# Kernel optimization log

Hardware: AMD Instinct MI355X
Metric: run time of the kernel (lower is better)

Reference implementation:

```python
import jax, jax.numpy as jnp
import numpy as np


def setup_inputs() -> dict:
    key = jax.random.key(0)
    k1, k2, k3 = jax.random.split(key, 3)
    B, Cin, Cout, K, H, W = 4, 64, 64, 3, 160, 160
    inputs = jax.random.normal(k1, (B, Cin, H, W), dtype=jnp.float32)
    # fractional dilation rates in [1, 3]
    rate_map = 1.0 + 2.0 * jax.random.uniform(k2, (B, 1, H, W), dtype=jnp.float32)
    # xavier-uniform-ish init
    limit = float(np.sqrt(6.0 / (Cin * K * K + Cout * K * K)))
    weight = jax.random.uniform(k3, (Cout, Cin, K, K), dtype=jnp.float32,
                                minval=-limit, maxval=limit)
    bias = jnp.zeros((Cout,), dtype=jnp.float32)
    return {"inputs": inputs, "weight": weight, "rate_map": rate_map,
            "bias": bias, "stride_h": 1, "stride_w": 1}


def _pdconv2d(inputs, weight, rate_map, bias, stride_h, stride_w):
    """Perspective (fractional, per-pixel) dilated conv with same padding.

    For each output pixel, the KxK taps are placed at center + offset*rate,
    where rate comes from rate_map and may be fractional -> bilinear sampling
    with zeros outside the image.
    """
    B, C, H, W = inputs.shape
    O, _, K, _ = weight.shape
    HO = (H + stride_h - 1) // stride_h
    WO = (W + stride_w - 1) // stride_w

    rate = rate_map[:, 0, ::stride_h, ::stride_w]  # [B,HO,WO]
    cy = (jnp.arange(HO) * stride_h).astype(jnp.float32)
    cx = (jnp.arange(WO) * stride_w).astype(jnp.float32)
    off = jnp.arange(K, dtype=jnp.float32) - (K - 1) / 2.0  # centered taps

    # sampling coords [B,HO,WO,K,K]
    sy = cy[None, :, None, None, None] + off[None, None, None, :, None] * rate[:, :, :, None, None]
    sx = cx[None, None, :, None, None] + off[None, None, None, None, :] * rate[:, :, :, None, None]
    sy = jnp.broadcast_to(sy, (B, HO, WO, K, K))
    sx = jnpp = jnp.broadcast_to(sx, (B, HO, WO, K, K))
    sx = jnp_p = sx  # no-op alias (keeps names clear)

    y0 = jnp.floor(sy)
    x0 = jnp.floor(sx)
    wy = sy - y0  # bilinear weights
    wx = sx - x0
    y0i = y0.astype(jnp.int32)
    x0i = x0.astype(jnp.int32)

    img = inputs.reshape(B, C, H * W)

    def gather(idx):  # idx [B,HO,WO,K,K] -> [B,C,HO,WO,K,K]
        return jax.vmap(lambda im, ix: jnp.take(im, ix, axis=-1))(img, idx)

    acc = jnp.zeros((B, C, HO, WO, K, K), dtype=inputs.dtype)
    corners = [(0, 0, (1 - wy) * (1 - wx)), (0, 1, (1 - wy) * wx),
               (1, 0, wy * (1 - wx)), (1, 1, wy * wx)]
    for dy, dx, cw in corners:
        yy = y0i + dy
        xx = x0i + dx
        valid = (yy >= 0) & (yy < H) & (xx >= 0) & (xx < W)
        idx = jnp.clip(yy, 0, H - 1) * W + jnp.clip(xx, 0, W - 1)
        w = (cw * valid.astype(inputs.dtype))[:, None]  # [B,1,HO,WO,K,K]
        acc = acc + gather(idx) * w

    # [B,C,HO,WO,K,K] x [O,C,K,K] -> [B,O,HO,WO]
    out = jnp.einsum('bchwkl,ockl->bohw', acc, weight)
    return out + bias[None, :, None, None]


def reference(inputs, weight, rate_map, bias, stride_h, stride_w):
    return _pdconv2d(inputs, weight, rate_map, bias, stride_h, stride_w)
```

## Files before the change

kernel.cpp:

```cpp
#include <hip/hip_runtime.h>
#include <hip/hip_bf16.h>

#define NB   4
#define CIN  64
#define COUT 64
#define HH   160
#define WW   160
#define HW   (HH * WW)

#define RT   8
#define CT   22
#define RS   72
#define HIN_SHORTS (RT * CT * RS)

typedef __attribute__((ext_vector_type(8))) short bf16x8;
typedef __attribute__((ext_vector_type(4))) float f32x4;
typedef __attribute__((ext_vector_type(2))) float f32x2;
typedef __attribute__((ext_vector_type(4))) unsigned int u32x4;

static __device__ __forceinline__ short f2bf(float v) {
    return __builtin_bit_cast(short, __float2bfloat16(v));
}

__global__ void wtf_kernel(const float* __restrict__ w, short* __restrict__ wtf) {
    int i = blockIdx.x * 256 + threadIdx.x;
    if (i < 36864) {
        const int j  = i & 7;
        const int l  = (i >> 3) & 63;
        const int mt = (i >> 9) & 3;
        const int ks = (i >> 11) & 1;
        const int t  = i >> 12;
        const int o  = 16 * mt + (l & 15);
        const int c  = 32 * ks + 8 * (l >> 4) + j;
        wtf[i] = f2bf(w[(o * CIN + c) * 9 + t]);
    }
}

__global__ __launch_bounds__(256) void tin_kernel(const float* __restrict__ in,
                                                  short* __restrict__ tin) {
    const int cpx = gridDim.x >> 3;
    const int wb  = (blockIdx.x & 7) * cpx + (blockIdx.x >> 3);
    const int gid = wb * 256 + threadIdx.x;
    if (gid >= NB * HW) return;
    const int b  = gid / HW;
    const int hw = gid - b * HW;
    const float* src = in + (size_t)b * CIN * HW + hw;
    short* dst = tin + (size_t)gid * CIN;
#pragma unroll
    for (int chunk = 0; chunk < 4; ++chunk) {
        union { u32x4 v; short s[8]; } p0, p1;
#pragma unroll
        for (int cc = 0; cc < 8; ++cc)
            p0.s[cc] = f2bf(src[(size_t)(chunk * 16 + cc) * HW]);
#pragma unroll
        for (int cc = 0; cc < 8; ++cc)
            p1.s[cc] = f2bf(src[(size_t)(chunk * 16 + 8 + cc) * HW]);
        *(u32x4*)(dst + chunk * 16)     = p0.v;
        *(u32x4*)(dst + chunk * 16 + 8) = p1.v;
    }
}

static __device__ __forceinline__ void consume_tap(
    const u32x4 v00, const u32x4 v01, const u32x4 v10, const u32x4 v11,
    const float c00, const float c01, const float c10, const float c11,
    const bf16x8 wf0, const bf16x8 wf1, const bf16x8 wf2, const bf16x8 wf3,
    f32x4 acc[4])
{
    union { bf16x8 v; unsigned u[4]; } pf;
#pragma unroll
    for (int wd = 0; wd < 4; ++wd) {
        f32x2 s;
        {
            const unsigned u0 = v00[wd];
            const f32x2 xv = { __builtin_bit_cast(float, u0 << 16),
                               __builtin_bit_cast(float, u0 & 0xffff0000u) };
            s = c00 * xv;
        }
        {
            const unsigned u0 = v01[wd];
            const f32x2 xv = { __builtin_bit_cast(float, u0 << 16),
                               __builtin_bit_cast(float, u0 & 0xffff0000u) };
            s += c01 * xv;
        }
        {
            const unsigned u0 = v10[wd];
            const f32x2 xv = { __builtin_bit_cast(float, u0 << 16),
                               __builtin_bit_cast(float, u0 & 0xffff0000u) };
            s += c10 * xv;
        }
        {
            const unsigned u0 = v11[wd];
            const f32x2 xv = { __builtin_bit_cast(float, u0 << 16),
                               __builtin_bit_cast(float, u0 & 0xffff0000u) };
            s += c11 * xv;
        }
        unsigned r;
        asm("v_cvt_pk_bf16_f32 %0, %1, %2" : "=v"(r) : "v"(s.x), "v"(s.y));
        pf.u[wd] = r;
    }
    acc[0] = __builtin_amdgcn_mfma_f32_16x16x32_bf16(wf0, pf.v, acc[0], 0, 0, 0);
    acc[1] = __builtin_amdgcn_mfma_f32_16x16x32_bf16(wf1, pf.v, acc[1], 0, 0, 0);
    acc[2] = __builtin_amdgcn_mfma_f32_16x16x32_bf16(wf2, pf.v, acc[2], 0, 0, 0);
    acc[3] = __builtin_amdgcn_mfma_f32_16x16x32_bf16(wf3, pf.v, acc[3], 0, 0, 0);
}

__global__ __launch_bounds__(256, 4) void pdconv_tile_kernel(
    const short* __restrict__ tin,
    const short* __restrict__ wtf,
    const float* __restrict__ rate_map,
    const float* __restrict__ bias,
    float* __restrict__ out)
{
    __shared__ short hin[HIN_SHORTS];
    __shared__ float red[2][64][17];

    const int tid  = threadIdx.x;
    const int wave = tid >> 6;
    const int lane = tid & 63;
    const int px   = lane & 15;
    const int g    = lane >> 4;
    const int r    = wave >> 1;
    const int th   = wave & 1;

    const int cpx = gridDim.x >> 3;
    const int bid = (blockIdx.x & 7) * cpx + (blockIdx.x >> 3);

    const int b   = bid / 800;
    const int rem = bid - b * 800;
    const int rr  = rem / 10;
    const int cc  = rem - rr * 10;
    const int oy  = 2 * rr - 3;
    const int ox  = 16 * cc - 3;

    const short* ib = tin + (size_t)b * HW * CIN;
#pragma unroll
    for (int it = 0; it < 6; ++it) {
        const int idx = it * 256 + tid;
        if (idx < RT * CT * 8) {
            const int rec = idx >> 3;
            const int cp  = idx & 7;
            const int ty  = rec / CT;
            const int tx  = rec - ty * CT;
            const int gy  = min(max(oy + ty, 0), HH - 1);
            const int gx  = min(max(ox + tx, 0), WW - 1);
            const u32x4 v = *(const u32x4*)(ib + ((size_t)gy * WW + gx) * CIN + cp * 8);
            *(u32x4*)(hin + rec * RS + cp * 8) = v;
        }
    }

    const int row = 2 * rr + r;
    const int x   = 16 * cc + px;
    const float rate = rate_map[b * HW + row * WW + x];
    const float fy = (float)row, fx = (float)x;

    const short* wtb = wtf + lane * 8;

    f32x4 acc[4];
#pragma unroll
    for (int mt = 0; mt < 4; ++mt) acc[mt] = (f32x4){0.f, 0.f, 0.f, 0.f};

    __syncthreads();

#define DO_TAP(T) do {                                                       \
    const int gky = (T) / 3, gkx = (T) - 3 * gky;                            \
    const float gsy = fy + (float)(gky - 1) * rate;                          \
    const float gsx = fx + (float)(gkx - 1) * rate;                          \
    const float gy0f = floorf(gsy), gx0f = floorf(gsx);                      \
    const float gwy = gsy - gy0f, gwx = gsx - gx0f;                          \
    const int gy0 = (int)gy0f, gx0 = (int)gx0f;                              \
    const float gomwy = 1.0f - gwy, gomwx = 1.0f - gwx;                      \
    const float gvy0 = (gy0 >= 0 && gy0 < HH) ? 1.0f : 0.0f;                 \
    const float gvy1 = (gy0 + 1 >= 0 && gy0 + 1 < HH) ? 1.0f : 0.0f;         \
    const float gvx0 = (gx0 >= 0 && gx0 < WW) ? 1.0f : 0.0f;                 \
    const float gvx1 = (gx0 + 1 >= 0 && gx0 + 1 < WW) ? 1.0f : 0.0f;         \
    const float c00 = gomwy * gomwx * gvy0 * gvx0;                           \
    const float c01 = gomwy * gwx   * gvy0 * gvx1;                           \
    const float c10 = gwy   * gomwx * gvy1 * gvx0;                           \
    const float c11 = gwy   * gwx   * gvy1 * gvx1;                           \
    const short* hk = hin + ((gy0 - oy) * CT + (gx0 - ox)) * RS              \
                          + 32 * th + 8 * g;                                 \
    const u32x4 v00 = *(const u32x4*)(hk);                                   \
    const u32x4 v01 = *(const u32x4*)(hk + RS);                              \
    const u32x4 v10 = *(const u32x4*)(hk + CT * RS);                         \
    const u32x4 v11 = *(const u32x4*)(hk + (CT + 1) * RS);                   \
    const short* wb = wtb + (size_t)(((T) * 2 + th) * 4) * 512;              \
    const bf16x8 wf0 = *(const bf16x8*)(wb);                                 \
    const bf16x8 wf1 = *(const bf16x8*)(wb + 512);                           \
    const bf16x8 wf2 = *(const bf16x8*)(wb + 1024);                          \
    const bf16x8 wf3 = *(const bf16x8*)(wb + 1536);                          \
    consume_tap(v00, v01, v10, v11, c00, c01, c10, c11,                      \
                wf0, wf1, wf2, wf3, acc);                                    \
} while (0)

    DO_TAP(0); DO_TAP(1); DO_TAP(2); DO_TAP(3); DO_TAP(4);
    DO_TAP(5); DO_TAP(6); DO_TAP(7); DO_TAP(8);
#undef DO_TAP

    if (th == 1) {
#pragma unroll
        for (int mt = 0; mt < 4; ++mt)
#pragma unroll
            for (int j = 0; j < 4; ++j)
                red[r][lane][4 * mt + j] = acc[mt][j];
    }
    __syncthreads();
    if (th == 0) {
        float* op = out + (size_t)b * COUT * HW + row * WW + 16 * cc + px;
#pragma unroll
        for (int mt = 0; mt < 4; ++mt) {
            const f32x4 bv = *(const f32x4*)(bias + 16 * mt + 4 * g);
#pragma unroll
            for (int j = 0; j < 4; ++j) {
                const int o = 16 * mt + 4 * g + j;
                op[(size_t)o * HW] = acc[mt][j] + red[r][lane][4 * mt + j]
                                   + bv[j];
            }
        }
    }
}

__global__ void wt2_kernel(const float* __restrict__ w, short* __restrict__ wt2) {
    int i = blockIdx.x * 256 + threadIdx.x;
    if (i < 9 * COUT * CIN) {
        int c = i & 63, o = (i >> 6) & 63, t = i >> 12;
        wt2[i] = f2bf(w[(o * CIN + c) * 9 + t]);
    }
}

__global__ __launch_bounds__(256) void pdconv_mfma_kernel(
    const float* __restrict__ in, const short* __restrict__ wt2,
    const float* __restrict__ rate_map, const float* __restrict__ bias,
    float* __restrict__ out)
{
    const int tid = threadIdx.x, wave = tid >> 6, lane = tid & 63;
    const int px = lane & 15, g = lane >> 4;
    const int cpx = gridDim.x >> 3;
    const int bid = (blockIdx.x & 7) * cpx + (blockIdx.x >> 3);
    const int base = bid * 64 + wave * 16;
    const int b = base / HW, pix0 = base - b * HW;
    const int y = pix0 / WW, x0 = pix0 - y * WW, x = x0 + px;
    const float rate = rate_map[base + px];
    const float fy = (float)y, fx = (float)x;
    f32x4 acc[4];
#pragma unroll
    for (int mt = 0; mt < 4; ++mt) acc[mt] = (f32x4){0.f, 0.f, 0.f, 0.f};
    const float* img  = in + (size_t)b * CIN * HW;
    const float* imgg = img + (size_t)g * 8 * HW;
#pragma unroll 1
    for (int t = 0; t < 9; ++t) {
        const int ky = t / 3, kx = t - 3 * ky;
        const float sy = fy + (float)(ky - 1) * rate;
        const float sx = fx + (float)(kx - 1) * rate;
        const float y0f = floorf(sy), x0f = floorf(sx);
        const float wy = sy - y0f, wx = sx - x0f;
        const int y0 = (int)y0f, x0i = (int)x0f, y1 = y0 + 1, x1 = x0i + 1;
        const float omwy = 1.0f - wy, omwx = 1.0f - wx;
        const float vy0 = (y0 >= 0 && y0 < HH) ? 1.0f : 0.0f;
        const float vy1 = (y1 >= 0 && y1 < HH) ? 1.0f : 0.0f;
        const float vx0 = (x0i >= 0 && x0i < WW) ? 1.0f : 0.0f;
        const float vx1 = (x1 >= 0 && x1 < WW) ? 1.0f : 0.0f;
        const float c00 = omwy * omwx * vy0 * vx0, c01 = omwy * wx * vy0 * vx1;
        const float c10 = wy * omwx * vy1 * vx0,  c11 = wy * wx * vy1 * vx1;
        const int cy0 = min(max(y0, 0), HH - 1), cy1 = min(max(y1, 0), HH - 1);
        const int cx0 = min(max(x0i, 0), WW - 1), cx1 = min(max(x1, 0), WW - 1);
        const int i00 = cy0 * WW + cx0, i01 = cy0 * WW + cx1;
        const int i10 = cy1 * WW + cx0, i11 = cy1 * WW + cx1;
#pragma unroll
        for (int ks = 0; ks < 2; ++ks) {
            bf16x8 wf[4];
#pragma unroll
            for (int mt = 0; mt < 4; ++mt)
                wf[mt] = *(const bf16x8*)(wt2 +
                          ((t * COUT + 16 * mt + px) * CIN + 32 * ks + 8 * g));
            float a[8];
#pragma unroll
            for (int j = 0; j < 8; ++j) {
                const float* ch = imgg + (size_t)(32 * ks + j) * HW;
                a[j] = c00 * ch[i00] + c01 * ch[i01] + c10 * ch[i10] + c11 * ch[i11];
            }
            union { bf16x8 v; short s[8]; } pf;
#pragma unroll
            for (int j = 0; j < 8; ++j) pf.s[j] = f2bf(a[j]);
#pragma unroll
            for (int mt = 0; mt < 4; ++mt)
                acc[mt] = __builtin_amdgcn_mfma_f32_16x16x32_bf16(
                              wf[mt], pf.v, acc[mt], 0, 0, 0);
        }
    }
    float* op = out + (size_t)b * COUT * HW + pix0 + px;
#pragma unroll
    for (int mt = 0; mt < 4; ++mt)
#pragma unroll
        for (int r = 0; r < 4; ++r) {
            const int o = 16 * mt + 4 * g + r;
            op[(size_t)o * HW] = acc[mt][r] + bias[o];
        }
}

extern "C" void kernel_launch(void* const* d_in, const int* in_sizes, int n_in,
                              void* d_out, int out_size, void* d_ws, size_t ws_size,
                              hipStream_t stream) {
    (void)in_sizes; (void)n_in; (void)out_size;
    const float* in   = (const float*)d_in[0];
    const float* w    = (const float*)d_in[1];
    const float* rm   = (const float*)d_in[2];
    const float* bias = (const float*)d_in[3];
    float* out = (float*)d_out;

    const size_t WTF_BYTES = 36864 * sizeof(short);
    const size_t TIN_BYTES = (size_t)NB * HW * CIN * sizeof(short);

    if (ws_size >= WTF_BYTES + TIN_BYTES) {
        short* wtf = (short*)d_ws;
        short* tin = (short*)((char*)d_ws + WTF_BYTES);
        hipLaunchKernelGGL(wtf_kernel, dim3(144), dim3(256), 0, stream, w, wtf);
        hipLaunchKernelGGL(tin_kernel, dim3((NB * HW) / 256), dim3(256),
                           0, stream, in, tin);
        const int nblocks = NB * 80 * 10;
        hipLaunchKernelGGL(pdconv_tile_kernel, dim3(nblocks), dim3(256), 0,
                           stream, tin, wtf, rm, bias, out);
    } else {
        short* wt2 = (short*)d_ws;
        hipLaunchKernelGGL(wt2_kernel, dim3(144), dim3(256), 0, stream, w, wt2);
        hipLaunchKernelGGL(pdconv_mfma_kernel, dim3((NB * HW) / 64), dim3(256),
                           0, stream, in, wt2, rm, bias, out);
    }
}
```

Before: 46.91 us.

## Merge prep kernels and preload all tap weights into registers before halo load

Folds the weight-reformat kernel and the input-transpose kernel into one prep kernel, saving a launch. In the main tile kernel, all 36 bf16x8 weight fragments are loaded into registers up front, overlapping the LDS halo fill, instead of being fetched from global memory per tap. An empty asm forces the loads to complete early. This costs about 144 extra VGPRs, so launch bounds drop from 4 to 2 blocks per CU, which reduces occupancy in exchange for taking weight-load latency off the tap loop.

```diff
diff --git a/kernel.cpp b/kernel.cpp
--- a/kernel.cpp
+++ b/kernel.cpp
@@ -22,8 +22,11 @@
     return __builtin_bit_cast(short, __float2bfloat16(v));
 }
 
-__global__ void wtf_kernel(const float* __restrict__ w, short* __restrict__ wtf) {
-    int i = blockIdx.x * 256 + threadIdx.x;
+__global__ __launch_bounds__(256) void prep_kernel(
+    const float* __restrict__ in,  short* __restrict__ tin,
+    const float* __restrict__ w,   short* __restrict__ wtf)
+{
+    const int i = blockIdx.x * 256 + threadIdx.x;
     if (i < 36864) {
         const int j  = i & 7;
         const int l  = (i >> 3) & 63;
@@ -34,10 +37,7 @@
         const int c  = 32 * ks + 8 * (l >> 4) + j;
         wtf[i] = f2bf(w[(o * CIN + c) * 9 + t]);
     }
-}
-
-__global__ __launch_bounds__(256) void tin_kernel(const float* __restrict__ in,
-                                                  short* __restrict__ tin) {
+
     const int cpx = gridDim.x >> 3;
     const int wb  = (blockIdx.x & 7) * cpx + (blockIdx.x >> 3);
     const int gid = wb * 256 + threadIdx.x;
@@ -104,7 +104,7 @@
     acc[3] = __builtin_amdgcn_mfma_f32_16x16x32_bf16(wf3, pf.v, acc[3], 0, 0, 0);
 }
 
-__global__ __launch_bounds__(256, 4) void pdconv_tile_kernel(
+__global__ __launch_bounds__(256, 2) void pdconv_tile_kernel(
     const short* __restrict__ tin,
     const short* __restrict__ wtf,
     const float* __restrict__ rate_map,
@@ -131,6 +131,15 @@
     const int cc  = rem - rr * 10;
     const int oy  = 2 * rr - 3;
     const int ox  = 16 * cc - 3;
+
+    const short* wtb = wtf + lane * 8;
+    union { bf16x8 v; u32x4 u; } wreg[36];
+#pragma unroll
+    for (int t = 0; t < 9; ++t)
+#pragma unroll
+        for (int mt = 0; mt < 4; ++mt)
+            wreg[t * 4 + mt].v = *(const bf16x8*)(wtb +
+                (size_t)((t * 2 + th) * 4 + mt) * 512);
 
     const short* ib = tin + (size_t)b * HW * CIN;
 #pragma unroll
@@ -148,12 +157,15 @@
         }
     }
 
+#pragma unroll
+    for (int i = 0; i < 36; ++i)
+        asm volatile("" :: "v"(wreg[i].u[0]), "v"(wreg[i].u[1]),
+                           "v"(wreg[i].u[2]), "v"(wreg[i].u[3]));
+
     const int row = 2 * rr + r;
     const int x   = 16 * cc + px;
     const float rate = rate_map[b * HW + row * WW + x];
     const float fy = (float)row, fx = (float)x;
-
-    const short* wtb = wtf + lane * 8;
 
     f32x4 acc[4];
 #pragma unroll
@@ -183,13 +195,9 @@
     const u32x4 v01 = *(const u32x4*)(hk + RS);                              \
     const u32x4 v10 = *(const u32x4*)(hk + CT * RS);                         \
     const u32x4 v11 = *(const u32x4*)(hk + (CT + 1) * RS);                   \
-    const short* wb = wtb + (size_t)(((T) * 2 + th) * 4) * 512;              \
-    const bf16x8 wf0 = *(const bf16x8*)(wb);                                 \
-    const bf16x8 wf1 = *(const bf16x8*)(wb + 512);                           \
-    const bf16x8 wf2 = *(const bf16x8*)(wb + 1024);                          \
-    const bf16x8 wf3 = *(const bf16x8*)(wb + 1536);                          \
     consume_tap(v00, v01, v10, v11, c00, c01, c10, c11,                      \
-                wf0, wf1, wf2, wf3, acc);                                    \
+                wreg[(T) * 4 + 0].v, wreg[(T) * 4 + 1].v,                    \
+                wreg[(T) * 4 + 2].v, wreg[(T) * 4 + 3].v, acc);              \
 } while (0)
 
     DO_TAP(0); DO_TAP(1); DO_TAP(2); DO_TAP(3); DO_TAP(4);
@@ -313,9 +321,8 @@
     if (ws_size >= WTF_BYTES + TIN_BYTES) {
         short* wtf = (short*)d_ws;
         short* tin = (short*)((char*)d_ws + WTF_BYTES);
-        hipLaunchKernelGGL(wtf_kernel, dim3(144), dim3(256), 0, stream, w, wtf);
-        hipLaunchKernelGGL(tin_kernel, dim3((NB * HW) / 256), dim3(256),
-                           0, stream, in, tin);
+        hipLaunchKernelGGL(prep_kernel, dim3((NB * HW) / 256), dim3(256),
+                           0, stream, in, tin, w, wtf);
         const int nblocks = NB * 80 * 10;
         hipLaunchKernelGGL(pdconv_tile_kernel, dim3(nblocks), dim3(256), 0,
                            stream, tin, wtf, rm, bias, out);
```

Result: slower. 54.69 us (+16.6%).
